# Kernel tuning notes

Hardware: AMD Instinct MI355X
Metric: run time of the kernel (lower is better)

Reference implementation:

```python
import jax, jax.numpy as jnp
import numpy as np

N, H, T, E, L = 10000, 512, 4, 40000, 2
TIMESTEPS = (2, 2)  # layer_timesteps


def setup_inputs() -> dict:
    key = jax.random.key(0)
    ks = jax.random.split(key, 10)
    s = 1.0 / np.sqrt(H)
    u = lambda k, shape: jax.random.uniform(k, shape, jnp.float32, -s, s)
    return {
        "x": jax.random.normal(ks[0], (N, H), jnp.float32),
        "edges": jax.random.randint(ks[1], (T, E, 2), 0, N),  # (src, tgt)
        "W_msg": u(ks[2], (L, T, H, H)),   # torch Linear weight [out, in]
        "b_msg": u(ks[3], (L, T, H)),
        "W_ih": u(ks[4], (L, 3 * H, H)),   # GRUCell input weights (r,z,n)
        "W_hh": u(ks[5], (L, 3 * H, H)),
        "b_ih": u(ks[6], (L, 3 * H)),
        "b_hh": u(ks[7], (L, 3 * H)),
        "fc_W": u(ks[8], (H, H)),
        "fc_b": u(ks[9], (H,)),
    }


def _gru_cell(x, h, W_ih, W_hh, b_ih, b_hh):
    # torch.nn.GRUCell math
    gi = x @ W_ih.T + b_ih  # [N, 3H]
    gh = h @ W_hh.T + b_hh
    i_r, i_z, i_n = jnp.split(gi, 3, axis=-1)
    h_r, h_z, h_n = jnp.split(gh, 3, axis=-1)
    r = jax.nn.sigmoid(i_r + h_r)
    z = jax.nn.sigmoid(i_z + h_z)
    n = jnp.tanh(i_n + r * h_n)
    return (1.0 - z) * n + z * h


def reference(x, edges, W_msg, b_msg, W_ih, W_hh, b_ih, b_hh, fc_W, fc_b):
    # dropout layers run in eval mode (identity)
    targets = edges[:, :, 1].reshape(-1)  # [T*E], concat order matches torch loop
    sources = edges[:, :, 0]              # [T, E]
    h = x
    for layer in range(L):
        for _ in range(TIMESTEPS[layer]):
            src_states = h[sources]  # [T, E, H] gather
            # per-edge-type Linear: y = x @ W.T + b
            msgs = jnp.einsum('teh,tkh->tek', src_states, W_msg[layer]) \
                   + b_msg[layer][:, None, :]
            incoming = jax.ops.segment_sum(msgs.reshape(-1, H), targets,
                                           num_segments=N)  # scatter_add
            h = _gru_cell(incoming, h, W_ih[layer], W_hh[layer],
                          b_ih[layer], b_hh[layer])
    out = h @ fc_W.T + fc_b          # [N, H]
    graph_repr = jnp.max(out, axis=0)  # max-pool over nodes -> [H]
    return graph_repr
```

## Files before the change

### kernel.cpp

```cpp
#include <hip/hip_runtime.h>
#include <hip/hip_bf16.h>


#define NN 10000
#define HD 512
#define NT 4
#define NE 40000
#define CAP 24
#define GYROWS 80

typedef __bf16 bf16x8 __attribute__((ext_vector_type(8)));
typedef float f32x4 __attribute__((ext_vector_type(4)));
union V16 { int4 i; bf16x8 b; };

typedef __attribute__((address_space(1))) const unsigned int gu32;
typedef __attribute__((address_space(3))) unsigned int lu32;
__device__ __forceinline__ void gll16(const void* g, void* l) {
    __builtin_amdgcn_global_load_lds((gu32*)g, (lu32*)l, 16, 0, 0);
}

__device__ __forceinline__ float bfl(__bf16 v) { return (float)v; }

__device__ __forceinline__ int4 cvt8(const float* __restrict__ s) {
    float4 v0 = *(const float4*)s, v1 = *(const float4*)(s + 4);
    V16 o;
    o.b[0] = (__bf16)v0.x; o.b[1] = (__bf16)v0.y; o.b[2] = (__bf16)v0.z; o.b[3] = (__bf16)v0.w;
    o.b[4] = (__bf16)v1.x; o.b[5] = (__bf16)v1.y; o.b[6] = (__bf16)v1.z; o.b[7] = (__bf16)v1.w;
    return o.i;
}

__device__ __forceinline__ void pk_decode(int rem, int KTbits, int& col, int& kk) {
    int ct = rem >> (KTbits + 9);
    int r2 = rem & ((1 << (KTbits + 9)) - 1);
    int kt = r2 >> 9, s = r2 & 511;
    int lane = s & 63;
    col = ct * 128 + ((s >> 8) << 6) + (((s >> 6) & 3) << 4) + (lane & 15);
    kk = kt * 32 + ((lane >> 4) & 3) * 8;
}

__global__ void prep_all(const float* __restrict__ Wmsg, const float* __restrict__ Wih,
                         const float* __restrict__ Whh, const float* __restrict__ fcW,
                         const float* __restrict__ x, const int* __restrict__ edges,
                         int4* __restrict__ WmPK, int4* __restrict__ WrznhPK,
                         int4* __restrict__ WfPK,
                         __hip_bfloat16* __restrict__ ab,
                         int* __restrict__ bcnt, int* __restrict__ bins) {
    int blk = blockIdx.x, tid = threadIdx.x;
    if (blk < 1024) {
        int g = blk * 256 + tid;
        int l = g >> 17, rem = g & 131071;
        int col, kk; pk_decode(rem, 4, col, kk);
        WmPK[g] = cvt8(Wmsg + (size_t)l * 1048576 + (size_t)col * 512 + kk);
        return;
    }
    blk -= 1024;
    if (blk < 2048) {
        int g = blk * 256 + tid;
        int l = g >> 18, rem = g & 262143;
        int col, kk; pk_decode(rem, 5, col, kk);
        int gate = (col >> 4) & 3;
        int hcol = ((col >> 7) * 2 + ((col >> 6) & 1)) * 16 + (col & 15);
        int4 v = make_int4(0, 0, 0, 0);
        if (kk < 512) {
            if (gate < 3) v = cvt8(Wih + (size_t)l * 786432 + (size_t)(gate * 512 + hcol) * 512 + kk);
        } else {
            if (gate < 2) v = cvt8(Whh + (size_t)l * 786432 + (size_t)(gate * 512 + hcol) * 512 + (kk - 512));
            else if (gate == 3) v = cvt8(Whh + (size_t)l * 786432 + (size_t)(1024 + hcol) * 512 + (kk - 512));
        }
        WrznhPK[g] = v;
        return;
    }
    blk -= 2048;
    if (blk < 128) {
        int g = blk * 256 + tid;
        int col, kk; pk_decode(g, 4, col, kk);
        WfPK[g] = cvt8(fcW + (size_t)col * 512 + kk);
        return;
    }
    blk -= 128;
    if (blk < 5000) {
        int i = blk * 1024 + tid * 4;
        float4 v = *(const float4*)(x + i);
        int m = i >> 9, c = i & 511;
        __hip_bfloat16 o[4] = {__float2bfloat16(v.x), __float2bfloat16(v.y),
                               __float2bfloat16(v.z), __float2bfloat16(v.w)};
        *(ulong1*)(ab + (size_t)m * 1024 + 512 + c) = *(ulong1*)o;
        return;
    }
    blk -= 5000;
    {
        int i = blk * 256 + tid;
        if (i >= NT * NE) return;
        int src = edges[2 * i], tgt = edges[2 * i + 1];
        int t = i / NE;
        int b = tgt * NT + t;
        int pos = atomicAdd(&bcnt[b], 1);
        if (pos < CAP) bins[(size_t)b * CAP + pos] = src;
    }
}

__global__ __launch_bounds__(256) void gather_msum(
    const int* __restrict__ bins, const int* __restrict__ bcnt,
    const float* __restrict__ bm, const __hip_bfloat16* __restrict__ Msg,
    __hip_bfloat16* __restrict__ inc) {
    int wave = threadIdx.x >> 6, lane = threadIdx.x & 63;
    int n = blockIdx.x * 4 + wave;
    int co = lane * 8;
    float acc[8] = {0, 0, 0, 0, 0, 0, 0, 0};
#pragma unroll
    for (int t = 0; t < NT; ++t) {
        int bi = n * NT + t;
        int cnt = bcnt[bi]; if (cnt > CAP) cnt = CAP;
        const int* bl = bins + (size_t)bi * CAP;
        for (int e = 0; e < cnt; ++e) {
            int src = bl[e];
            V16 v; v.i = *(const int4*)(Msg + (size_t)src * 2048 + t * 512 + co);
#pragma unroll
            for (int k = 0; k < 8; ++k) acc[k] += (float)v.b[k];
        }
        float4 b0 = *(const float4*)(bm + t * 512 + co);
        float4 b1 = *(const float4*)(bm + t * 512 + co + 4);
        float fc = (float)cnt;
        acc[0] += fc * b0.x; acc[1] += fc * b0.y; acc[2] += fc * b0.z; acc[3] += fc * b0.w;
        acc[4] += fc * b1.x; acc[5] += fc * b1.y; acc[6] += fc * b1.z; acc[7] += fc * b1.w;
    }
    V16 o;
#pragma unroll
    for (int k = 0; k < 8; ++k) o.b[k] = (__bf16)acc[k];
    *(int4*)(inc + (size_t)n * 1024 + co) = o.i;
}

__device__ __forceinline__ unsigned fenc(float f) {
    unsigned b = __float_as_uint(f);
    return b ^ (((int)b >> 31) | 0x80000000u);
}
__device__ __forceinline__ float fdec(unsigned u) {
    unsigned b = (u & 0x80000000u) ? (u ^ 0x80000000u) : ~u;
    return __uint_as_float(b);
}

template<int MODE>
__global__ __launch_bounds__(256, 3) void gemm(
    const __hip_bfloat16* __restrict__ A, int lda, int K,
    const int4* __restrict__ Wpk,
    const float* __restrict__ b0, const float* __restrict__ b1,
    __hip_bfloat16* __restrict__ obf, int ldo,
    unsigned* __restrict__ om) {
    __shared__ int4 sA4[3][1024];
    __shared__ unsigned sm[128];
    __hip_bfloat16* lds = (__hip_bfloat16*)sA4;
    float2* ldsZ = (float2*)sA4;

    const int NB = (MODE == 3) ? 4 : 16;
    int bid = blockIdx.x;
    int xcd = bid & 7, kq = bid >> 3;
    int bcol = kq % NB;
    int brow = xcd + 8 * (kq / NB);
    int m0 = brow * 128, n0 = bcol * 128;

    int tid = threadIdx.x;
    int lane = tid & 63, wave = tid >> 6;
    int wr = wave >> 1, wc = wave & 1;
    int lm = lane & 15, quad = lane >> 4;
    int qx = (lm >> 1) & 3;

    const int KT32 = K >> 5;
    const int KT = K >> 6;
    const int kend = KT;
    const int4* Wp = Wpk + ((size_t)bcol * KT32 << 9) + wc * 256 + lane;

    auto issueA = [&](int kt, int p) {
        int k0 = kt << 6;
#pragma unroll
        for (int it = 0; it < 4; ++it) {
            int idx = it * 256 + tid;
            int s = idx >> 9, rem = idx & 511;
            int row = rem >> 2;
            int kc = (rem & 3) ^ ((row >> 1) & 3);
            int gm = m0 + row; gm = gm < NN ? gm : NN - 1;
            gll16(A + (size_t)gm * lda + k0 + s * 32 + kc * 8,
                  (__hip_bfloat16*)(sA4[p]) + idx * 8);
        }
    };
    auto loadB = [&](int kt, int4 (&bb)[2][4]) {
#pragma unroll
        for (int s = 0; s < 2; ++s) {
            const int4* wn = Wp + ((size_t)(2 * kt + s) << 9);
#pragma unroll
            for (int j = 0; j < 4; ++j) bb[s][j] = wn[j * 64];
        }
    };

    f32x4 acc[4][4] = {};
    int4 bb0[2][4], bb1[2][4];
    issueA(0, 0);
    issueA(1, 1);
    loadB(0, bb0);

    auto ktbody = [&](int kt, int4 (&bbCur)[2][4], int4 (&bbNxt)[2][4]) {
        int p = kt % 3;
        if (kt + 1 < kend) loadB(kt + 1, bbNxt);
        __builtin_amdgcn_sched_barrier(0);
        if (kt + 1 < kend) __builtin_amdgcn_s_waitcnt(0x4F74);
        else               __builtin_amdgcn_s_waitcnt(0x0F78);
        __builtin_amdgcn_s_barrier();
        __builtin_amdgcn_sched_barrier(0);
        if (kt + 2 < kend) issueA(kt + 2, (kt + 2) % 3);
#pragma unroll
        for (int s = 0; s < 2; ++s) {
            V16 a[4];
#pragma unroll
            for (int i = 0; i < 4; ++i)
                a[i].i = sA4[p][s * 512 + (wr * 64 + i * 16 + lm) * 4 + (quad ^ qx)];
#pragma unroll
            for (int i = 0; i < 4; ++i)
#pragma unroll
                for (int j = 0; j < 4; ++j) {
                    if (MODE == 1) {
                        if (j == 2 && kt >= 8) continue;
                        if (j == 3 && kt < 8) continue;
                    }
                    V16 b; b.i = bbCur[s][j];
                    acc[i][j] = __builtin_amdgcn_mfma_f32_16x16x32_bf16(a[i].b, b.b, acc[i][j], 0, 0, 0);
                }
        }
        __builtin_amdgcn_sched_barrier(0);
    };

    for (int k2 = 0; k2 < kend; k2 += 2) {
        ktbody(k2, bb0, bb1);
        ktbody(k2 + 1, bb1, bb0);
    }

    if (MODE == 0) {
        __syncthreads();
#pragma unroll
        for (int ph = 0; ph < 2; ++ph) {
            if (wr == ph) {
#pragma unroll
                for (int j = 0; j < 4; ++j) {
                    int c = wc * 64 + j * 16 + lm;
#pragma unroll
                    for (int i = 0; i < 4; ++i)
#pragma unroll
                        for (int r = 0; r < 4; ++r)
                            lds[(i * 16 + quad * 4 + r) * 128 + c] = __float2bfloat16(acc[i][j][r]);
                }
            }
            __syncthreads();
#pragma unroll
            for (int q = 0; q < 4; ++q) {
                int idx = q * 256 + tid;
                int rl = idx >> 4, c16 = idx & 15;
                int m = m0 + ph * 64 + rl;
                if (m < NN)
                    *(int4*)(obf + (size_t)m * ldo + n0 + c16 * 8) =
                        *(const int4*)(lds + rl * 128 + c16 * 8);
            }
            __syncthreads();
        }
    } else if (MODE == 1) {
        __syncthreads();
        int c32 = wc * 16 + lm;
        int hcol = bcol * 32 + c32;
        float rb = b0[hcol] + b1[hcol];
        float zb = b0[512 + hcol] + b1[512 + hcol];
        float ib = b0[1024 + hcol];
        float hb = b1[1024 + hcol];
#pragma unroll
        for (int i = 0; i < 4; ++i)
#pragma unroll
            for (int r = 0; r < 4; ++r) {
                int rloc = wr * 64 + i * 16 + quad * 4 + r;
                float rr = 1.f / (1.f + __expf(-(acc[i][0][r] + rb)));
                float zz = 1.f / (1.f + __expf(-(acc[i][1][r] + zb)));
                float nx = (acc[i][2][r] + ib) + rr * (acc[i][3][r] + hb);
                float n = 1.f - 2.f / (__expf(2.f * nx) + 1.f);
                ldsZ[rloc * 34 + c32] = make_float2((1.f - zz) * n, zz);
            }
        __syncthreads();
#pragma unroll
        for (int q = 0; q < 4; ++q) {
            int idx = q * 256 + tid;
            int rl = idx >> 3, c4 = (idx & 7) * 4;
            int m = m0 + rl;
            if (m < NN) {
                ulong1 hraw = *(const ulong1*)(A + (size_t)m * lda + 512 + bcol * 32 + c4);
                const __bf16* hb4 = (const __bf16*)&hraw;
                const float2* pz = ldsZ + rl * 34 + c4;
                __hip_bfloat16 ob[4];
#pragma unroll
                for (int e = 0; e < 4; ++e) {
                    float2 az = pz[e];
                    ob[e] = __float2bfloat16(az.x + az.y * bfl(hb4[e]));
                }
                *(ulong1*)(obf + (size_t)m * ldo + bcol * 32 + c4) = *(ulong1*)ob;
            }
        }
    } else {
        if (tid < 128) sm[tid] = 0;
        __syncthreads();
#pragma unroll
        for (int j = 0; j < 4; ++j) {
            int c = wc * 64 + j * 16 + lm;
            float bias = b0[n0 + c];
            float mx = -INFINITY;
#pragma unroll
            for (int i = 0; i < 4; ++i) {
                int r0 = m0 + wr * 64 + i * 16 + quad * 4;
#pragma unroll
                for (int r = 0; r < 4; ++r) {
                    int m = r0 + r;
                    if (m < NN) mx = fmaxf(mx, acc[i][j][r] + bias);
                }
            }
            atomicMax(&sm[c], fenc(mx));
        }
        __syncthreads();
        if (tid < 128) atomicMax(&om[n0 + tid], sm[tid]);
    }
}

__global__ void writeout(const unsigned* __restrict__ om, float* __restrict__ o) {
    int c = threadIdx.x;
    o[c] = fdec(om[c]);
}

extern "C" void kernel_launch(void* const* d_in, const int* in_sizes, int n_in,
                              void* d_out, int out_size, void* d_ws, size_t ws_size,
                              hipStream_t stream) {
    (void)in_sizes; (void)n_in; (void)out_size; (void)ws_size;
    const float* x    = (const float*)d_in[0];
    const int*   edges= (const int*)d_in[1];
    const float* Wmsg = (const float*)d_in[2];
    const float* bmsg = (const float*)d_in[3];
    const float* Wih  = (const float*)d_in[4];
    const float* Whh  = (const float*)d_in[5];
    const float* bih  = (const float*)d_in[6];
    const float* bhh  = (const float*)d_in[7];
    const float* fcW  = (const float*)d_in[8];
    const float* fcb  = (const float*)d_in[9];
    float* out = (float*)d_out;

    char* ws = (char*)d_ws;
    size_t off = 0;
    auto alloc = [&](size_t bytes) -> void* {
        void* p = ws + off; off += (bytes + 255) & ~(size_t)255; return p;
    };
    __hip_bfloat16* abA  = (__hip_bfloat16*)alloc((size_t)NN * 1024 * 2);
    __hip_bfloat16* abB  = (__hip_bfloat16*)alloc((size_t)NN * 1024 * 2);
    int*            bcnt = (int*)alloc((size_t)NN * NT * 4);
    int*            bins = (int*)alloc((size_t)NN * NT * CAP * 4);
    unsigned*       om   = (unsigned*)alloc(HD * 4);
    int4*           WmPK   = (int4*)alloc((size_t)2 * 131072 * 16);
    int4*           WrznhPK= (int4*)alloc((size_t)2 * 262144 * 16);
    int4*           WfPK   = (int4*)alloc((size_t)32768 * 16);
    __hip_bfloat16* Msg  = (__hip_bfloat16*)alloc((size_t)NN * 2048 * 2);

    hipMemsetAsync(bcnt, 0, (size_t)NN * NT * 4, stream);
    hipMemsetAsync(om, 0, HD * 4, stream);
    prep_all<<<1024 + 2048 + 128 + 5000 + 625, 256, 0, stream>>>(
        Wmsg, Wih, Whh, fcW, x, edges, WmPK, WrznhPK, WfPK, abA, bcnt, bins);

    for (int s = 0; s < 4; ++s) {
        int layer = s >> 1;
        __hip_bfloat16* cur = (s & 1) ? abB : abA;
        __hip_bfloat16* nxt = (s & 1) ? abA : abB;
        const int4* Wm = WmPK + (size_t)layer * 131072;
        const int4* Wz = WrznhPK + (size_t)layer * 262144;
        const float* bm = bmsg + (size_t)layer * 2048;
        const float* bi = bih + (size_t)layer * 1536;
        const float* bh = bhh + (size_t)layer * 1536;

        gemm<0><<<16 * GYROWS, 256, 0, stream>>>(cur + 512, 1024, 512, Wm,
            nullptr, nullptr, Msg, 2048, nullptr);
        gather_msum<<<NN / 4, 256, 0, stream>>>(bins, bcnt, bm, Msg, cur);
        gemm<1><<<16 * GYROWS, 256, 0, stream>>>(cur, 1024, 1024, Wz,
            bi, bh, nxt + 512, 1024, nullptr);
    }
    gemm<3><<<4 * GYROWS, 256, 0, stream>>>(abA + 512, 1024, 512, WfPK,
        fcb, nullptr, nullptr, 0, om);
    writeout<<<1, 512, 0, stream>>>(om, out);
}
```

Measured before the change: 558.9 us.

## Gather-then-transform: aggregate source states per edge type before message GEMM

The message step now sums gathered source hidden states per (target, edge type) into a [N, 4*512] buffer first. It then runs a single K=2048 GEMM against the concatenated per-type message weights, adding count-weighted biases in the epilogue. This replaces the N x 2048-wide message GEMM followed by a gather of bf16 messages. The GEMM output width drops from 2048 to 512, though its K grows to 2048. The gather now writes a 2048-wide bf16 buffer and rounds partial sums to bf16 before the matmul, which may change numerics slightly.

```diff
diff --git a/kernel.cpp b/kernel.cpp
--- a/kernel.cpp
+++ b/kernel.cpp
@@ -41,7 +41,7 @@
 __global__ void prep_all(const float* __restrict__ Wmsg, const float* __restrict__ Wih,
                          const float* __restrict__ Whh, const float* __restrict__ fcW,
                          const float* __restrict__ x, const int* __restrict__ edges,
-                         int4* __restrict__ WmPK, int4* __restrict__ WrznhPK,
+                         int4* __restrict__ WiPK, int4* __restrict__ WrznhPK,
                          int4* __restrict__ WfPK,
                          __hip_bfloat16* __restrict__ ab,
                          int* __restrict__ bcnt, int* __restrict__ bins) {
@@ -49,8 +49,9 @@
     if (blk < 1024) {
         int g = blk * 256 + tid;
         int l = g >> 17, rem = g & 131071;
-        int col, kk; pk_decode(rem, 4, col, kk);
-        WmPK[g] = cvt8(Wmsg + (size_t)l * 1048576 + (size_t)col * 512 + kk);
+        int col, kk; pk_decode(rem, 6, col, kk);
+        WiPK[g] = cvt8(Wmsg + (size_t)l * 1048576 + (size_t)(kk >> 9) * 262144
+                       + (size_t)col * 512 + (kk & 511));
         return;
     }
     blk -= 1024;
@@ -99,35 +100,30 @@
     }
 }
 
-__global__ __launch_bounds__(256) void gather_msum(
+__global__ __launch_bounds__(256) void gather_h(
     const int* __restrict__ bins, const int* __restrict__ bcnt,
-    const float* __restrict__ bm, const __hip_bfloat16* __restrict__ Msg,
-    __hip_bfloat16* __restrict__ inc) {
+    const __hip_bfloat16* __restrict__ h,
+    __hip_bfloat16* __restrict__ S) {
     int wave = threadIdx.x >> 6, lane = threadIdx.x & 63;
     int n = blockIdx.x * 4 + wave;
     int co = lane * 8;
-    float acc[8] = {0, 0, 0, 0, 0, 0, 0, 0};
 #pragma unroll
     for (int t = 0; t < NT; ++t) {
         int bi = n * NT + t;
         int cnt = bcnt[bi]; if (cnt > CAP) cnt = CAP;
         const int* bl = bins + (size_t)bi * CAP;
+        float acc[8] = {0, 0, 0, 0, 0, 0, 0, 0};
         for (int e = 0; e < cnt; ++e) {
             int src = bl[e];
-            V16 v; v.i = *(const int4*)(Msg + (size_t)src * 2048 + t * 512 + co);
+            V16 v; v.i = *(const int4*)(h + (size_t)src * 1024 + co);
 #pragma unroll
             for (int k = 0; k < 8; ++k) acc[k] += (float)v.b[k];
         }
-        float4 b0 = *(const float4*)(bm + t * 512 + co);
-        float4 b1 = *(const float4*)(bm + t * 512 + co + 4);
-        float fc = (float)cnt;
-        acc[0] += fc * b0.x; acc[1] += fc * b0.y; acc[2] += fc * b0.z; acc[3] += fc * b0.w;
-        acc[4] += fc * b1.x; acc[5] += fc * b1.y; acc[6] += fc * b1.z; acc[7] += fc * b1.w;
-    }
-    V16 o;
-#pragma unroll
-    for (int k = 0; k < 8; ++k) o.b[k] = (__bf16)acc[k];
-    *(int4*)(inc + (size_t)n * 1024 + co) = o.i;
+        V16 o;
+#pragma unroll
+        for (int k = 0; k < 8; ++k) o.b[k] = (__bf16)acc[k];
+        *(int4*)(S + (size_t)n * 2048 + t * 512 + co) = o.i;
+    }
 }
 
 __device__ __forceinline__ unsigned fenc(float f) {
@@ -145,13 +141,13 @@
     const int4* __restrict__ Wpk,
     const float* __restrict__ b0, const float* __restrict__ b1,
     __hip_bfloat16* __restrict__ obf, int ldo,
-    unsigned* __restrict__ om) {
+    const int* __restrict__ bcnt, unsigned* __restrict__ om) {
     __shared__ int4 sA4[3][1024];
     __shared__ unsigned sm[128];
     __hip_bfloat16* lds = (__hip_bfloat16*)sA4;
     float2* ldsZ = (float2*)sA4;
 
-    const int NB = (MODE == 3) ? 4 : 16;
+    const int NB = (MODE >= 2) ? 4 : 16;
     int bid = blockIdx.x;
     int xcd = bid & 7, kq = bid >> 3;
     int bcol = kq % NB;
@@ -232,8 +228,46 @@
         ktbody(k2 + 1, bb1, bb0);
     }
 
-    if (MODE == 0) {
+    if (MODE == 0 || MODE == 2) {
         __syncthreads();
+        if (MODE == 2) {
+            int* ldsCnt = (int*)((char*)sA4 + 40960);
+            float* ldsBm = (float*)((char*)sA4 + 43008);
+            if (tid < 128) {
+                int m = m0 + tid;
+                int4 c4 = make_int4(0, 0, 0, 0);
+                if (m < NN) c4 = *(const int4*)(bcnt + (size_t)m * 4);
+                c4.x = c4.x > CAP ? CAP : c4.x;
+                c4.y = c4.y > CAP ? CAP : c4.y;
+                c4.z = c4.z > CAP ? CAP : c4.z;
+                c4.w = c4.w > CAP ? CAP : c4.w;
+                *(int4*)(ldsCnt + tid * 4) = c4;
+            } else if (tid < 256) {
+                int i2 = tid - 128;
+                int t = i2 >> 5, cq = (i2 & 31) << 2;
+                *(float4*)(ldsBm + t * 128 + cq) = *(const float4*)(b0 + t * 512 + n0 + cq);
+            }
+            __syncthreads();
+            float bmv[4][4];
+#pragma unroll
+            for (int j = 0; j < 4; ++j) {
+                int c = wc * 64 + j * 16 + lm;
+#pragma unroll
+                for (int t = 0; t < 4; ++t) bmv[j][t] = ldsBm[t * 128 + c];
+            }
+#pragma unroll
+            for (int i = 0; i < 4; ++i)
+#pragma unroll
+                for (int r = 0; r < 4; ++r) {
+                    int rloc = wr * 64 + i * 16 + quad * 4 + r;
+                    int4 cc = *(const int4*)(ldsCnt + rloc * 4);
+#pragma unroll
+                    for (int j = 0; j < 4; ++j)
+                        acc[i][j][r] += (float)cc.x * bmv[j][0] + (float)cc.y * bmv[j][1]
+                                      + (float)cc.z * bmv[j][2] + (float)cc.w * bmv[j][3];
+                }
+            __syncthreads();
+        }
 #pragma unroll
         for (int ph = 0; ph < 2; ++ph) {
             if (wr == ph) {
@@ -352,33 +386,33 @@
     int*            bcnt = (int*)alloc((size_t)NN * NT * 4);
     int*            bins = (int*)alloc((size_t)NN * NT * CAP * 4);
     unsigned*       om   = (unsigned*)alloc(HD * 4);
-    int4*           WmPK   = (int4*)alloc((size_t)2 * 131072 * 16);
+    int4*           WiPK   = (int4*)alloc((size_t)2 * 131072 * 16);
     int4*           WrznhPK= (int4*)alloc((size_t)2 * 262144 * 16);
     int4*           WfPK   = (int4*)alloc((size_t)32768 * 16);
-    __hip_bfloat16* Msg  = (__hip_bfloat16*)alloc((size_t)NN * 2048 * 2);
+    __hip_bfloat16* S    = (__hip_bfloat16*)alloc((size_t)NN * 2048 * 2);
 
     hipMemsetAsync(bcnt, 0, (size_t)NN * NT * 4, stream);
     hipMemsetAsync(om, 0, HD * 4, stream);
     prep_all<<<1024 + 2048 + 128 + 5000 + 625, 256, 0, stream>>>(
-        Wmsg, Wih, Whh, fcW, x, edges, WmPK, WrznhPK, WfPK, abA, bcnt, bins);
+        Wmsg, Wih, Whh, fcW, x, edges, WiPK, WrznhPK, WfPK, abA, bcnt, bins);
 
     for (int s = 0; s < 4; ++s) {
         int layer = s >> 1;
         __hip_bfloat16* cur = (s & 1) ? abB : abA;
         __hip_bfloat16* nxt = (s & 1) ? abA : abB;
-        const int4* Wm = WmPK + (size_t)layer * 131072;
+        const int4* Wi = WiPK + (size_t)layer * 131072;
         const int4* Wz = WrznhPK + (size_t)layer * 262144;
         const float* bm = bmsg + (size_t)layer * 2048;
         const float* bi = bih + (size_t)layer * 1536;
         const float* bh = bhh + (size_t)layer * 1536;
 
-        gemm<0><<<16 * GYROWS, 256, 0, stream>>>(cur + 512, 1024, 512, Wm,
-            nullptr, nullptr, Msg, 2048, nullptr);
-        gather_msum<<<NN / 4, 256, 0, stream>>>(bins, bcnt, bm, Msg, cur);
+        gather_h<<<NN / 4, 256, 0, stream>>>(bins, bcnt, cur + 512, S);
+        gemm<2><<<4 * GYROWS, 256, 0, stream>>>(S, 2048, 2048, Wi,
+            bm, nullptr, cur, 1024, bcnt, nullptr);
         gemm<1><<<16 * GYROWS, 256, 0, stream>>>(cur, 1024, 1024, Wz,
-            bi, bh, nxt + 512, 1024, nullptr);
+            bi, bh, nxt + 512, 1024, nullptr, nullptr);
     }
     gemm<3><<<4 * GYROWS, 256, 0, stream>>>(abA + 512, 1024, 512, WfPK,
-        fcb, nullptr, nullptr, 0, om);
+        fcb, nullptr, nullptr, 0, nullptr, om);
     writeout<<<1, 512, 0, stream>>>(om, out);
 }
```

Result: slower. 691.4 us (+23.7%).

## Widen GRU gemm blocks to 512 threads covering two column tiles

Applied to the files above, without the earlier changes.

The GRU gate GEMM (MODE 1) now launches half as many blocks with 512 threads each. Each block computes two adjacent 32-column hidden tiles that share one staged A tile in LDS, so A is loaded from global memory half as often. The epilogue is split into two LDS passes, one per column tile, with extra barriers, and the per-thread A-load count and waitcnt are adjusted. The trade-off is lower occupancy (2 blocks per CU), more synchronisation, and fewer blocks in the grid.

```diff
diff --git a/kernel.cpp b/kernel.cpp
--- a/kernel.cpp
+++ b/kernel.cpp
@@ -140,7 +140,7 @@
 }
 
 template<int MODE>
-__global__ __launch_bounds__(256, 3) void gemm(
+__global__ __launch_bounds__((MODE == 1) ? 512 : 256, (MODE == 1) ? 2 : 3) void gemm(
     const __hip_bfloat16* __restrict__ A, int lda, int K,
     const int4* __restrict__ Wpk,
     const float* __restrict__ b0, const float* __restrict__ b1,
@@ -151,7 +151,8 @@
     __hip_bfloat16* lds = (__hip_bfloat16*)sA4;
     float2* ldsZ = (float2*)sA4;
 
-    const int NB = (MODE == 3) ? 4 : 16;
+    const int NB = (MODE == 3) ? 4 : ((MODE == 1) ? 8 : 16);
+    const int NTH = (MODE == 1) ? 512 : 256;
     int bid = blockIdx.x;
     int xcd = bid & 7, kq = bid >> 3;
     int bcol = kq % NB;
@@ -160,20 +161,23 @@
 
     int tid = threadIdx.x;
     int lane = tid & 63, wave = tid >> 6;
-    int wr = wave >> 1, wc = wave & 1;
+    int wr, wc, ct_off;
+    if (MODE == 1) { wr = wave >> 2; ct_off = (wave >> 1) & 1; wc = wave & 1; }
+    else           { wr = wave >> 1; ct_off = 0;               wc = wave & 1; }
     int lm = lane & 15, quad = lane >> 4;
     int qx = (lm >> 1) & 3;
 
     const int KT32 = K >> 5;
     const int KT = K >> 6;
     const int kend = KT;
-    const int4* Wp = Wpk + ((size_t)bcol * KT32 << 9) + wc * 256 + lane;
+    int ct = (MODE == 1) ? (bcol * 2 + ct_off) : bcol;
+    const int4* Wp = Wpk + ((size_t)ct * KT32 << 9) + wc * 256 + lane;
 
     auto issueA = [&](int kt, int p) {
         int k0 = kt << 6;
 #pragma unroll
-        for (int it = 0; it < 4; ++it) {
-            int idx = it * 256 + tid;
+        for (int it = 0; it < 1024 / NTH; ++it) {
+            int idx = it * NTH + tid;
             int s = idx >> 9, rem = idx & 511;
             int row = rem >> 2;
             int kc = (rem & 3) ^ ((row >> 1) & 3);
@@ -201,7 +205,7 @@
         int p = kt % 3;
         if (kt + 1 < kend) loadB(kt + 1, bbNxt);
         __builtin_amdgcn_sched_barrier(0);
-        if (kt + 1 < kend) __builtin_amdgcn_s_waitcnt(0x4F74);
+        if (kt + 1 < kend) __builtin_amdgcn_s_waitcnt((MODE == 1) ? 0x4F72 : 0x4F74);
         else               __builtin_amdgcn_s_waitcnt(0x0F78);
         __builtin_amdgcn_s_barrier();
         __builtin_amdgcn_sched_barrier(0);
@@ -261,41 +265,48 @@
         }
     } else if (MODE == 1) {
         __syncthreads();
-        int c32 = wc * 16 + lm;
-        int hcol = bcol * 32 + c32;
+        int hcol = ct * 32 + wc * 16 + lm;
         float rb = b0[hcol] + b1[hcol];
         float zb = b0[512 + hcol] + b1[512 + hcol];
         float ib = b0[1024 + hcol];
         float hb = b1[1024 + hcol];
 #pragma unroll
-        for (int i = 0; i < 4; ++i)
-#pragma unroll
-            for (int r = 0; r < 4; ++r) {
-                int rloc = wr * 64 + i * 16 + quad * 4 + r;
-                float rr = 1.f / (1.f + __expf(-(acc[i][0][r] + rb)));
-                float zz = 1.f / (1.f + __expf(-(acc[i][1][r] + zb)));
-                float nx = (acc[i][2][r] + ib) + rr * (acc[i][3][r] + hb);
-                float n = 1.f - 2.f / (__expf(2.f * nx) + 1.f);
-                ldsZ[rloc * 34 + c32] = make_float2((1.f - zz) * n, zz);
-            }
-        __syncthreads();
-#pragma unroll
-        for (int q = 0; q < 4; ++q) {
-            int idx = q * 256 + tid;
-            int rl = idx >> 3, c4 = (idx & 7) * 4;
-            int m = m0 + rl;
-            if (m < NN) {
-                ulong1 hraw = *(const ulong1*)(A + (size_t)m * lda + 512 + bcol * 32 + c4);
-                const __bf16* hb4 = (const __bf16*)&hraw;
-                const float2* pz = ldsZ + rl * 34 + c4;
-                __hip_bfloat16 ob[4];
-#pragma unroll
-                for (int e = 0; e < 4; ++e) {
-                    float2 az = pz[e];
-                    ob[e] = __float2bfloat16(az.x + az.y * bfl(hb4[e]));
+        for (int g = 0; g < 2; ++g) {
+            if (ct_off == g) {
+                int c32 = wc * 16 + lm;
+#pragma unroll
+                for (int i = 0; i < 4; ++i)
+#pragma unroll
+                    for (int r = 0; r < 4; ++r) {
+                        int rloc = wr * 64 + i * 16 + quad * 4 + r;
+                        float rr = 1.f / (1.f + __expf(-(acc[i][0][r] + rb)));
+                        float zz = 1.f / (1.f + __expf(-(acc[i][1][r] + zb)));
+                        float nx = (acc[i][2][r] + ib) + rr * (acc[i][3][r] + hb);
+                        float n = 1.f - 2.f / (__expf(2.f * nx) + 1.f);
+                        ldsZ[rloc * 34 + c32] = make_float2((1.f - zz) * n, zz);
+                    }
+            }
+            __syncthreads();
+            int colb = bcol * 64 + g * 32;
+#pragma unroll
+            for (int q = 0; q < 2; ++q) {
+                int idx = q * 512 + tid;
+                int rl = idx >> 3, c4 = (idx & 7) * 4;
+                int m = m0 + rl;
+                if (m < NN) {
+                    ulong1 hraw = *(const ulong1*)(A + (size_t)m * lda + 512 + colb + c4);
+                    const __bf16* hb4 = (const __bf16*)&hraw;
+                    const float2* pz = ldsZ + rl * 34 + c4;
+                    __hip_bfloat16 ob[4];
+#pragma unroll
+                    for (int e = 0; e < 4; ++e) {
+                        float2 az = pz[e];
+                        ob[e] = __float2bfloat16(az.x + az.y * bfl(hb4[e]));
+                    }
+                    *(ulong1*)(obf + (size_t)m * ldo + colb + c4) = *(ulong1*)ob;
                 }
-                *(ulong1*)(obf + (size_t)m * ldo + bcol * 32 + c4) = *(ulong1*)ob;
-            }
+            }
+            __syncthreads();
         }
     } else {
         if (tid < 128) sm[tid] = 0;
@@ -375,7 +386,7 @@
         gemm<0><<<16 * GYROWS, 256, 0, stream>>>(cur + 512, 1024, 512, Wm,
             nullptr, nullptr, Msg, 2048, nullptr);
         gather_msum<<<NN / 4, 256, 0, stream>>>(bins, bcnt, bm, Msg, cur);
-        gemm<1><<<16 * GYROWS, 256, 0, stream>>>(cur, 1024, 1024, Wz,
+        gemm<1><<<8 * GYROWS, 512, 0, stream>>>(cur, 1024, 1024, Wz,
             bi, bh, nxt + 512, 1024, nullptr);
     }
     gemm<3><<<4 * GYROWS, 256, 0, stream>>>(abA + 512, 1024, 512, WfPK,
```

After: 690.5 us. 1.24x slower.
